# Kernel optimization log

Measured on AMD Instinct MI355X. Metric: run time of the kernel, lower is better.

The kernel has to match this reference:

```python
import jax, jax.numpy as jnp
import numpy as np

B, L = 16, 256
H, NH, NL = 512, 8, 6
NTOK = 10000
P, K = 4, 9          # parser layers, conv kernel size
DFF = 4 * H


def layernorm(x, s=None, b=None, eps=1e-5):
    m = x.mean(-1, keepdims=True)
    v = ((x - m) ** 2).mean(-1, keepdims=True)
    y = (x - m) * jax.lax.rsqrt(v + eps)
    if s is not None:
        y = y * s + b
    return y


def conv1d(h, w, b):
    # h: (B,L,C); w: (K,Cin,Cout); 'same' padding (K odd)
    pad = (K - 1) // 2
    return jax.lax.conv_general_dilated(
        h, w, (1,), [(pad, pad)], dimension_numbers=('NWC', 'WIO', 'NWC')) + b


def setup_inputs():
    key = jax.random.key(0)
    ks = iter(jax.random.split(key, 40))
    r = lambda shape, s=0.02: jax.random.normal(next(ks), shape, jnp.float32) * s
    return dict(
        x=jax.random.randint(next(ks), (B, L), 0, NTOK, jnp.int32),
        pos=jnp.tile(jnp.arange(L, dtype=jnp.int32), (B, 1)),
        emb=r((NTOK, H), 0.1),
        conv_w=r((P, K, H, H)), conv_b=jnp.zeros((P, H)),
        parent_w=r((H, H)), parent_b=jnp.zeros((H,)),
        child_w=r((H, H)), child_b=jnp.zeros((H,)),
        rel_w_param=r((NL, NH, 2), 0.1),
        qkv_w=r((NL, 3 * H, H)), qkv_b=jnp.zeros((NL, 3 * H)),
        out_w=r((NL, H, H)), out_b=jnp.zeros((NL, H)),
        ln1_s=jnp.ones((NL, H)), ln1_b=jnp.zeros((NL, H)),
        ln2_s=jnp.ones((NL, H)), ln2_b=jnp.zeros((NL, H)),
        ff1_w=r((NL, DFF, H)), ff1_b=jnp.zeros((NL, DFF)),
        ff2_w=r((NL, H, DFF)), ff2_b=jnp.zeros((NL, H)),
        norm_s=jnp.ones((H,)), norm_b=jnp.zeros((H,)),
        out_bias=jnp.zeros((NTOK,)),
    )


def _forward(x, floats):
    (emb, conv_w, conv_b, parent_w, parent_b, child_w, child_b, rel_w_param,
     qkv_w, qkv_b, out_w, out_b, ln1_s, ln1_b, ln2_s, ln2_b,
     ff1_w, ff1_b, ff2_w, ff2_b, norm_s, norm_b, out_bias) = floats
    mask = x != 0  # pad token index = 0
    DH = H // NH
    scale = H ** -0.5
    # ---- differentiable parser: Conv1d + LN(no affine) + Tanh stack ----
    h = emb[x]
    for i in range(P):
        h = jnp.where(mask[..., None], h, 0.0)
        h = jnp.tanh(layernorm(conv1d(h, conv_w[i], conv_b[i])))
    parent = h @ parent_w.T + parent_b
    child = h @ child_w.T + child_b
    logits = jnp.einsum('bid,bjd->bij', child, parent) * scale
    logits = jnp.where(mask[:, None, :], logits, -jnp.inf)
    # NB: source applies scaling twice (masked_fill then softmax(logits*scaling))
    p = jax.nn.softmax(logits * scale, axis=-1)  # (B,L,L) head distribution
    # ---- structural relations -> per-layer/per-head attention bias ----
    eye = jnp.eye(L, dtype=bool)
    head = jnp.where(eye, 0.0, p)
    child_rel = jnp.swapaxes(head, 1, 2)
    rel = jnp.stack([head, child_rel], axis=1)            # (B,2,L,L)
    rel_weight = jax.nn.softmax(rel_w_param, axis=-1)     # (NL,NH,2)
    dep = jnp.einsum('lhr,brij->lbhij', rel_weight, rel)  # (NL,B,NH,L,L)
    # ---- pre-LN transformer encoder with structural bias injection ----
    logvis = jnp.where(mask, 0.0, -jnp.inf)[:, None, None, :]  # key padding mask (log)
    h = emb[x]
    for i in range(NL):
        hn = layernorm(h, ln1_s[i], ln1_b[i])
        qkv = hn @ qkv_w[i].T + qkv_b[i]
        q, k, v = jnp.split(qkv, 3, axis=-1)
        split = lambda t: t.reshape(B, L, NH, DH).transpose(0, 2, 1, 3)
        q, k, v = split(q), split(k), split(v)
        att = jnp.einsum('bhid,bhjd->bhij', q, k) * (DH ** -0.5) + dep[i] + logvis
        att = jax.nn.softmax(att, axis=-1)
        ctx = jnp.einsum('bhij,bhjd->bhid', att, v).transpose(0, 2, 1, 3).reshape(B, L, H)
        h = h + ctx @ out_w[i].T + out_b[i]
        hn = layernorm(h, ln2_s[i], ln2_b[i])
        h = h + jax.nn.leaky_relu(hn @ ff1_w[i].T + ff1_b[i], 0.01) @ ff2_w[i].T + ff2_b[i]
    raw = layernorm(h, norm_s, norm_b)
    out = (raw @ emb.T + out_bias).reshape(B * L, NTOK)  # tied output embedding
    return out


def reference(x, pos, emb, conv_w, conv_b, parent_w, parent_b, child_w, child_b,
              rel_w_param, qkv_w, qkv_b, out_w, out_b, ln1_s, ln1_b, ln2_s, ln2_b,
              ff1_w, ff1_b, ff2_w, ff2_b, norm_s, norm_b, out_bias):
    floats = (emb, conv_w, conv_b, parent_w, parent_b, child_w, child_b, rel_w_param,
              qkv_w, qkv_b, out_w, out_b, ln1_s, ln1_b, ln2_s, ln2_b,
              ff1_w, ff1_b, ff2_w, ff2_b, norm_s, norm_b, out_bias)
    return _forward(x, floats)
```

## Files before the change

kernel.cpp:

```cpp
#include <hip/hip_runtime.h>
#include <hip/hip_bf16.h>


typedef unsigned short u16;
typedef unsigned char  u8;
typedef short short8 __attribute__((ext_vector_type(8)));
typedef float f32x4  __attribute__((ext_vector_type(4)));

static constexpr int CB=16, CL=256, CH=512, CNH=8, CDH=64, CNL=6;
static constexpr int CNTOK=10000, CP=4, CKS=9, CDFF=2048, CT=CB*CL;
static constexpr int NTOKP=10112;

__device__ __forceinline__ u16 f2b(float x){
    union { float f; unsigned u; } v; v.f = x;
    unsigned r = v.u + 0x7fffu + ((v.u >> 16) & 1u);
    return (u16)(r >> 16);
}
__device__ __forceinline__ float b2f(u16 u){
    union { unsigned u; float f; } v; v.u = ((unsigned)u) << 16; return v.f;
}
__device__ __forceinline__ unsigned pack2(float a, float b){
    return (unsigned)f2b(a) | ((unsigned)f2b(b) << 16);
}
__device__ __forceinline__ void gll16(const void* g, void* l){
    __builtin_amdgcn_global_load_lds(
        (__attribute__((address_space(1))) void*)g,
        (__attribute__((address_space(3))) void*)l, 16, 0, 0);
}

__global__ __launch_bounds__(256) void cvt_k(const float* __restrict__ in,
    u16* __restrict__ out, long n, long total)
{
    long i = ((long)blockIdx.x * 256 + threadIdx.x) * 8;
    if (i >= total) return;
    uint4 o;
    if (i < n) {
        float4 a = *(const float4*)(in + i);
        float4 b = *(const float4*)(in + i + 4);
        o.x = pack2(a.x, a.y); o.y = pack2(a.z, a.w);
        o.z = pack2(b.x, b.y); o.w = pack2(b.z, b.w);
    } else { o.x = o.y = o.z = o.w = 0u; }
    *(uint4*)(out + i) = o;
}

__global__ __launch_bounds__(256) void embed2_k(const int* __restrict__ x,
    const float* __restrict__ emb, float* __restrict__ h,
    u16* __restrict__ abuf, u8* __restrict__ maskb)
{
    int t = blockIdx.x, tid = threadIdx.x;
    int tok = x[t];
    if (tid == 0) maskb[t] = (tok != 0) ? 1 : 0;
    const float* e = emb + (size_t)tok * CH;
    float v0 = e[tid], v1 = e[tid + 256];
    float* hp = h + (size_t)t * CH;
    hp[tid] = v0; hp[tid + 256] = v1;
    u16* ap = abuf + (size_t)t * CH;
    ap[tid] = f2b(v0); ap[tid + 256] = f2b(v1);
}

template<bool INBF, bool AFFINE, bool DOTANH>
__global__ __launch_bounds__(256) void ln_k(const void* __restrict__ in,
    const float* __restrict__ s, const float* __restrict__ b, u16* __restrict__ out)
{
    int t = blockIdx.x, tid = threadIdx.x;
    float x0, x1;
    if (INBF) {
        const u16* row = (const u16*)in + (size_t)t * CH;
        x0 = b2f(row[tid]); x1 = b2f(row[tid + 256]);
    } else {
        const float* row = (const float*)in + (size_t)t * CH;
        x0 = row[tid]; x1 = row[tid + 256];
    }
    float sum = x0 + x1, sq = x0*x0 + x1*x1;
    #pragma unroll
    for (int o = 32; o; o >>= 1) { sum += __shfl_down(sum, o); sq += __shfl_down(sq, o); }
    __shared__ float rs[4], rq[4];
    int w = tid >> 6, lane = tid & 63;
    if (lane == 0) { rs[w] = sum; rq[w] = sq; }
    __syncthreads();
    sum = rs[0] + rs[1] + rs[2] + rs[3];
    sq  = rq[0] + rq[1] + rq[2] + rq[3];
    float mean = sum * (1.f/512.f);
    float var  = fmaxf(sq * (1.f/512.f) - mean*mean, 0.f);
    float rstd = rsqrtf(var + 1e-5f);
    float y0 = (x0 - mean) * rstd, y1 = (x1 - mean) * rstd;
    if (AFFINE) {
        y0 = y0 * s[tid]       + b[tid];
        y1 = y1 * s[tid + 256] + b[tid + 256];
    }
    if (DOTANH) { y0 = tanhf(y0); y1 = tanhf(y1); }
    u16* o = out + (size_t)t * CH;
    o[tid] = f2b(y0); o[tid + 256] = f2b(y1);
}

__global__ __launch_bounds__(256) void tp_conv(const float* __restrict__ src,
    u16* __restrict__ dst)
{
    __shared__ float tile[32][33];
    int z = blockIdx.z, p = z / 9, t = z % 9;
    int ci0 = blockIdx.y * 32, co0 = blockIdx.x * 32;
    int tx = threadIdx.x, ty = threadIdx.y;
    #pragma unroll
    for (int yy = 0; yy < 4; yy++) {
        int i = ty + yy*8;
        tile[i][tx] = src[((size_t)z*512 + ci0 + i)*512 + co0 + tx];
    }
    __syncthreads();
    #pragma unroll
    for (int yy = 0; yy < 4; yy++) {
        int i = ty + yy*8;
        dst[((size_t)p*512 + co0 + i)*4608 + (size_t)t*512 + ci0 + tx] = f2b(tile[tx][i]);
    }
}

template<int BM, bool CONV, int ACT, int OUT>
__global__ __launch_bounds__(256) void gemm2(
    const u16* __restrict__ A, const u16* __restrict__ B,
    const float* __restrict__ bias, void* __restrict__ Cv,
    const u8* __restrict__ mask,
    int M, int N, int K, float alpha, long sA, long sB, long sC, int swz)
{
    constexpr int MI = BM / 32;
    __shared__ __align__(16) u16 As[32 * BM];
    __shared__ __align__(16) u16 Bs[4096];

    int bx = blockIdx.x, by = blockIdx.y;
    if (swz) {
        int nwg = gridDim.x * gridDim.y;
        int bid = by * gridDim.x + bx;
        int s = (bid & 7) * (nwg >> 3) + (bid >> 3);
        bx = s % gridDim.x; by = s / gridDim.x;
    }
    const int tid  = threadIdx.x;
    const int lane = tid & 63, wave = tid >> 6;
    const int q = lane >> 4, ln = lane & 15;
    const int wm = wave >> 1, wn = wave & 1;
    const int m0 = by * BM, n0 = bx * 128;
    const int z  = blockIdx.z;
    A += (size_t)z * sA; B += (size_t)z * sB;

    f32x4 acc[MI][4];
    #pragma unroll
    for (int i = 0; i < MI; i++)
        #pragma unroll
        for (int j = 0; j < 4; j++)
            #pragma unroll
            for (int r = 0; r < 4; r++) acc[i][j][r] = 0.f;

    for (int k0 = 0; k0 < K; k0 += 32) {
        if (!CONV) {
            if (BM == 128) {
                #pragma unroll
                for (int t = 0; t < 2; t++) {
                    int c = wave + t*4;
                    int kq = c >> 1, rh = (c & 1) << 6;
                    gll16(A + (size_t)(m0 + rh + lane) * K + k0 + kq*8, As + c*512);
                }
            } else {
                gll16(A + (size_t)(m0 + lane) * K + k0 + wave*8, As + wave*512);
            }
        } else {
            int tap = k0 >> 9;
            int ci  = (k0 & 511) + wave*8;
            int gr  = m0 + lane;
            int bb  = gr >> 8;
            int l2  = (gr & 255) + tap - 4;
            bool ok = ((unsigned)l2 < 256u) && mask[(bb << 8) | l2];
            uint4 v; v.x = v.y = v.z = v.w = 0u;
            if (ok) v = *(const uint4*)(A + ((size_t)((bb << 8) | l2)) * CH + ci);
            *(uint4*)&As[wave*512 + lane*8] = v;
        }
        #pragma unroll
        for (int t = 0; t < 2; t++) {
            int c = wave + t*4;
            int kq = c >> 1, rh = (c & 1) << 6;
            gll16(B + (size_t)(n0 + rh + lane) * K + k0 + kq*8, Bs + c*512);
        }
        __syncthreads();
        short8 af[MI], bf[4];
        #pragma unroll
        for (int f = 0; f < MI; f++)
            af[f] = *(const short8*)&As[q*(BM*8) + (wm*(BM/2) + f*16 + ln)*8];
        #pragma unroll
        for (int g = 0; g < 4; g++)
            bf[g] = *(const short8*)&Bs[q*1024 + (wn*64 + g*16 + ln)*8];
        #pragma unroll
        for (int f = 0; f < MI; f++)
            #pragma unroll
            for (int g = 0; g < 4; g++)
                acc[f][g] = __builtin_amdgcn_mfma_f32_16x16x32_bf16(af[f], bf[g], acc[f][g], 0, 0, 0);
        __syncthreads();
    }
    float* Cf = (float*)Cv; u16* Cb = (u16*)Cv;
    #pragma unroll
    for (int f = 0; f < MI; f++) {
        int row0 = m0 + wm*(BM/2) + f*16 + q*4;
        #pragma unroll
        for (int g = 0; g < 4; g++) {
            int col = n0 + wn*64 + g*16 + ln;
            if (col < N) {
                #pragma unroll
                for (int r = 0; r < 4; r++) {
                    float v = acc[f][g][r] * alpha;
                    if (bias) v += bias[col];
                    if (ACT == 1) v = v > 0.f ? v : 0.01f * v;
                    size_t idx = (size_t)z * sC + (size_t)(row0 + r) * N + col;
                    if (OUT == 0)      Cf[idx] = v;
                    else if (OUT == 1) Cb[idx] = f2b(v);
                    else               Cf[idx] += v;
                }
            }
        }
    }
}

__global__ __launch_bounds__(256) void softmax_head(float* __restrict__ sc,
    const u8* __restrict__ mask)
{
    int bi = blockIdx.x;
    int b = bi >> 8, i = bi & 255;
    int j = threadIdx.x;
    float* rowp = sc + (size_t)bi * CL;
    bool valid = mask[(b << 8) | j] != 0;
    float v = valid ? rowp[j] : -1e30f;
    float mx = v;
    #pragma unroll
    for (int o = 32; o; o >>= 1) mx = fmaxf(mx, __shfl_down(mx, o));
    __shared__ float rm[4], rsum[4];
    int w = j >> 6, lane = j & 63;
    if (lane == 0) rm[w] = mx;
    __syncthreads();
    mx = fmaxf(fmaxf(rm[0], rm[1]), fmaxf(rm[2], rm[3]));
    float e = valid ? __expf(v - mx) : 0.f;
    float ssum = e;
    #pragma unroll
    for (int o = 32; o; o >>= 1) ssum += __shfl_down(ssum, o);
    if (lane == 0) rsum[w] = ssum;
    __syncthreads();
    ssum = rsum[0] + rsum[1] + rsum[2] + rsum[3];
    float r = e / fmaxf(ssum, 1e-30f);
    if (j == i) r = 0.f;
    rowp[j] = r;
}

__global__ __launch_bounds__(256) void attn_k(const u16* __restrict__ qkv,
    const float* __restrict__ head, const float* __restrict__ relw,
    const u8* __restrict__ mask, u16* __restrict__ ctx, int layer)
{
    __shared__ __align__(16) u16 Ks[CL * CDH];
    __shared__ __align__(16) u16 Vs[CL * CDH];
    int bx = blockIdx.x;
    int b = bx >> 4, hd = (bx >> 1) & 7, qh = bx & 1;
    int tid = threadIdx.x;

    #pragma unroll
    for (int r = 0; r < 8; r++) {
        int ef = tid + 256 * r;
        int j = ef >> 3, d8 = (ef & 7) * 8;
        const u16* ps = qkv + (size_t)(b*256 + j) * 1536 + 512 + hd*64 + d8;
        *(uint4*)&Ks[j*64 + d8] = *(const uint4*)ps;
        *(uint4*)&Vs[j*64 + d8] = *(const uint4*)(ps + 512);
    }

    int qi = qh * 128 + (tid >> 1);
    int half = tid & 1;
    float qv[CDH];
    {
        const u16* qp = qkv + (size_t)(b*256 + qi) * 1536 + hd*64;
        #pragma unroll
        for (int c = 0; c < 8; c++) {
            uint4 u = *(const uint4*)(qp + c*8);
            unsigned uu[4] = {u.x, u.y, u.z, u.w};
            #pragma unroll
            for (int p2 = 0; p2 < 4; p2++) {
                qv[c*8 + p2*2]     = b2f((u16)(uu[p2] & 0xffffu));
                qv[c*8 + p2*2 + 1] = b2f((u16)(uu[p2] >> 16));
            }
        }
    }
    float r0 = relw[((layer << 3) + hd) * 2 + 0];
    float r1 = relw[((layer << 3) + hd) * 2 + 1];
    float e0 = __expf(r0), e1 = __expf(r1);
    float w0 = e0 / (e0 + e1), w1 = 1.f - w0;

    __syncthreads();

    const float* h1 = head + ((size_t)b << 16) + ((size_t)qi << 8);
    const float* h2 = head + ((size_t)b << 16) + qi;
    const u8* mb = mask + (b << 8);

    float m = -1e30f, lsum = 0.f;
    float acc[CDH];
    #pragma unroll
    for (int d = 0; d < CDH; d++) acc[d] = 0.f;

    for (int jj = 0; jj < 128; jj++) {
        int j = half * 128 + jj;
        if (!mb[j]) continue;
        float dot = 0.f;
        #pragma unroll
        for (int d = 0; d < CDH; d++) dot += qv[d] * b2f(Ks[(j << 6) + d]);
        float s = dot * 0.125f + w0 * h1[j] + w1 * h2[(size_t)j << 8];
        float mn = fmaxf(m, s);
        float c = __expf(m - mn);
        float p = __expf(s - mn);
        lsum = lsum * c + p;
        #pragma unroll
        for (int d = 0; d < CDH; d++) acc[d] = acc[d] * c + p * b2f(Vs[(j << 6) + d]);
        m = mn;
    }
    {
        float mo = __shfl_xor(m, 1);
        float lo = __shfl_xor(lsum, 1);
        float M  = fmaxf(m, mo);
        float cs = __expf(m - M);
        float co = __expf(mo - M);
        lsum = lsum * cs + lo * co;
        #pragma unroll
        for (int d = 0; d < CDH; d++) {
            float ao = __shfl_xor(acc[d], 1);
            acc[d] = acc[d] * cs + ao * co;
        }
    }
    if (half == 0) {
        float inv = 1.f / fmaxf(lsum, 1e-30f);
        u16* cp = ctx + (size_t)(b*256 + qi) * CH + (hd << 6);
        #pragma unroll
        for (int d = 0; d < CDH; d++) cp[d] = f2b(acc[d] * inv);
    }
}

extern "C" void kernel_launch(void* const* d_in, const int* in_sizes, int n_in,
                              void* d_out, int out_size, void* d_ws, size_t ws_size,
                              hipStream_t stream)
{
    const int*   x        = (const int*)d_in[0];
    const float* emb      = (const float*)d_in[2];
    const float* conv_w   = (const float*)d_in[3];
    const float* conv_b   = (const float*)d_in[4];
    const float* parent_w = (const float*)d_in[5];
    const float* parent_b = (const float*)d_in[6];
    const float* child_w  = (const float*)d_in[7];
    const float* child_b  = (const float*)d_in[8];
    const float* rel_w    = (const float*)d_in[9];
    const float* qkv_w    = (const float*)d_in[10];
    const float* qkv_b    = (const float*)d_in[11];
    const float* out_w    = (const float*)d_in[12];
    const float* out_b    = (const float*)d_in[13];
    const float* ln1_s    = (const float*)d_in[14];
    const float* ln1_b    = (const float*)d_in[15];
    const float* ln2_s    = (const float*)d_in[16];
    const float* ln2_b    = (const float*)d_in[17];
    const float* ff1_w    = (const float*)d_in[18];
    const float* ff1_b    = (const float*)d_in[19];
    const float* ff2_w    = (const float*)d_in[20];
    const float* ff2_b    = (const float*)d_in[21];
    const float* norm_s   = (const float*)d_in[22];
    const float* norm_b   = (const float*)d_in[23];
    const float* out_bias = (const float*)d_in[24];

    float* ws = (float*)d_ws;
    float* h      = ws;
    float* headp  = ws + 2097152;
    u16*   abuf   = (u16*)(ws + 3145728);
    u16*   Rb     = (u16*)(ws + 4194304);
    u16*   qkvb   = Rb;
    u16*   parentb= Rb;
    u16*   childb = Rb + 2097152;
    u16*   convo  = Rb + 4194304;
    u16*   ctxb   = (u16*)(ws + 7340032);
    u16*   ff1b   = (u16*)(ws + 8388608);
    u16*   convwb = (u16*)(ws + 7340032);
    u8*    maskb  = (u8*)(ws + 12582912);
    u16*   ebf16  = (u16*)(ws + 12583936);
    u16*   qkvwb  = (u16*)(ws + 15172608);
    u16*   outwb  = (u16*)(ws + 17531904);
    u16*   ff1wb  = (u16*)(ws + 18318336);
    u16*   ff2wb  = (u16*)(ws + 21464064);
    u16*   parwb  = (u16*)(ws + 24609792);
    u16*   chlwb  = (u16*)(ws + 24740864);

    tp_conv<<<dim3(16,16,36), dim3(32,8), 0, stream>>>(conv_w, convwb);
    cvt_k<<<2528, 256, 0, stream>>>(emb,      ebf16, (long)CNTOK*CH, (long)NTOKP*CH);
    cvt_k<<<2304, 256, 0, stream>>>(qkv_w,    qkvwb, 4718592L, 4718592L);
    cvt_k<<< 768, 256, 0, stream>>>(out_w,    outwb, 1572864L, 1572864L);
    cvt_k<<<3072, 256, 0, stream>>>(ff1_w,    ff1wb, 6291456L, 6291456L);
    cvt_k<<<3072, 256, 0, stream>>>(ff2_w,    ff2wb, 6291456L, 6291456L);
    cvt_k<<< 128, 256, 0, stream>>>(parent_w, parwb,  262144L,  262144L);
    cvt_k<<< 128, 256, 0, stream>>>(child_w,  chlwb,  262144L,  262144L);

    embed2_k<<<CT, 256, 0, stream>>>(x, emb, h, abuf, maskb);

    for (int p = 0; p < CP; p++) {
        gemm2<64,true,0,1><<<dim3(4,64,1), 256, 0, stream>>>(
            abuf, convwb + (size_t)p*512*4608, conv_b + p*512, convo, maskb,
            CT, 512, 4608, 1.f, 0, 0, 0, 0);
        ln_k<true,false,true><<<CT, 256, 0, stream>>>(convo, nullptr, nullptr, abuf);
    }
    gemm2<64,false,0,1><<<dim3(4,64,1), 256, 0, stream>>>(
        abuf, parwb, parent_b, parentb, nullptr, CT, 512, 512, 1.f, 0, 0, 0, 0);
    gemm2<64,false,0,1><<<dim3(4,64,1), 256, 0, stream>>>(
        abuf, chlwb, child_b, childb, nullptr, CT, 512, 512, 1.f, 0, 0, 0, 0);
    gemm2<64,false,0,0><<<dim3(2,4,16), 256, 0, stream>>>(
        childb, parentb, nullptr, headp, nullptr, 256, 256, 512, 1.f/512.f,
        131072, 131072, 65536, 0);
    softmax_head<<<CT, 256, 0, stream>>>(headp, maskb);

    for (int l = 0; l < CNL; l++) {
        ln_k<false,true,false><<<CT, 256, 0, stream>>>(h, ln1_s + l*CH, ln1_b + l*CH, abuf);
        gemm2<128,false,0,1><<<dim3(12,32,1), 256, 0, stream>>>(
            abuf, qkvwb + (size_t)l*1536*512, qkv_b + l*1536, qkvb, nullptr,
            CT, 1536, 512, 1.f, 0, 0, 0, 0);
        attn_k<<<256, 256, 0, stream>>>(qkvb, headp, rel_w, maskb, ctxb, l);
        gemm2<64,false,0,2><<<dim3(4,64,1), 256, 0, stream>>>(
            ctxb, outwb + (size_t)l*512*512, out_b + l*512, h, nullptr,
            CT, 512, 512, 1.f, 0, 0, 0, 0);
        ln_k<false,true,false><<<CT, 256, 0, stream>>>(h, ln2_s + l*CH, ln2_b + l*CH, abuf);
        gemm2<128,false,1,1><<<dim3(16,32,1), 256, 0, stream>>>(
            abuf, ff1wb + (size_t)l*2048*512, ff1_b + l*2048, ff1b, nullptr,
            CT, 2048, 512, 1.f, 0, 0, 0, 0);
        gemm2<64,false,0,2><<<dim3(4,64,1), 256, 0, stream>>>(
            ff1b, ff2wb + (size_t)l*512*2048, ff2_b + l*512, h, nullptr,
            CT, 512, 2048, 1.f, 0, 0, 0, 0);
    }
    ln_k<false,true,false><<<CT, 256, 0, stream>>>(h, norm_s, norm_b, abuf);
    gemm2<128,false,0,0><<<dim3(79,32,1), 256, 0, stream>>>(
        abuf, ebf16, out_bias, d_out, nullptr, CT, CNTOK, 512, 1.f, 0, 0, 0, 1);
}
```

Measured before the change: 2.595 ms.

## Pad conv input, transpose head matrix, split-K residual GEMMs, column-major swizzle

The conv input now lives in a zero-padded per-batch buffer with masked rows zeroed at write time. The conv GEMM can then load A tiles with direct global-to-LDS copies, with no bounds or mask checks. The head matrix is transposed once so attention reads its second term contiguously instead of with a 256-float stride. The out-proj and FF2 GEMMs use 2-way split-K with atomic adds into the residual to double the block count. Several GEMMs also switch to a different block swizzle. The transposed head buffer borrows the output buffer as scratch, and the atomics make the summation order nondeterministic.

```diff
diff --git a/kernel.cpp b/kernel.cpp
--- a/kernel.cpp
+++ b/kernel.cpp
@@ -10,6 +10,7 @@
 static constexpr int CB=16, CL=256, CH=512, CNH=8, CDH=64, CNL=6;
 static constexpr int CNTOK=10000, CP=4, CKS=9, CDFF=2048, CT=CB*CL;
 static constexpr int NTOKP=10112;
+static constexpr int LP=264;
 
 __device__ __forceinline__ u16 f2b(float x){
     union { float f; unsigned u; } v; v.f = x;
@@ -45,22 +46,26 @@
 
 __global__ __launch_bounds__(256) void embed2_k(const int* __restrict__ x,
     const float* __restrict__ emb, float* __restrict__ h,
-    u16* __restrict__ abuf, u8* __restrict__ maskb)
+    u16* __restrict__ ppad, u8* __restrict__ maskb)
 {
     int t = blockIdx.x, tid = threadIdx.x;
     int tok = x[t];
-    if (tid == 0) maskb[t] = (tok != 0) ? 1 : 0;
+    bool mk = (tok != 0);
+    if (tid == 0) maskb[t] = mk ? 1 : 0;
     const float* e = emb + (size_t)tok * CH;
     float v0 = e[tid], v1 = e[tid + 256];
     float* hp = h + (size_t)t * CH;
     hp[tid] = v0; hp[tid + 256] = v1;
-    u16* ap = abuf + (size_t)t * CH;
-    ap[tid] = f2b(v0); ap[tid + 256] = f2b(v1);
-}
-
-template<bool INBF, bool AFFINE, bool DOTANH>
+    int pr = (t >> 8) * LP + 4 + (t & 255);
+    u16* ap = ppad + (size_t)pr * CH;
+    ap[tid]       = mk ? f2b(v0) : (u16)0;
+    ap[tid + 256] = mk ? f2b(v1) : (u16)0;
+}
+
+template<bool INBF, bool AFFINE, bool DOTANH, int OUTMODE>
 __global__ __launch_bounds__(256) void ln_k(const void* __restrict__ in,
-    const float* __restrict__ s, const float* __restrict__ b, u16* __restrict__ out)
+    const float* __restrict__ s, const float* __restrict__ b, u16* __restrict__ out,
+    const u8* __restrict__ mask)
 {
     int t = blockIdx.x, tid = threadIdx.x;
     float x0, x1;
@@ -89,8 +94,16 @@
         y1 = y1 * s[tid + 256] + b[tid + 256];
     }
     if (DOTANH) { y0 = tanhf(y0); y1 = tanhf(y1); }
-    u16* o = out + (size_t)t * CH;
-    o[tid] = f2b(y0); o[tid + 256] = f2b(y1);
+    if (OUTMODE == 0) {
+        u16* o = out + (size_t)t * CH;
+        o[tid] = f2b(y0); o[tid + 256] = f2b(y1);
+    } else {
+        bool mk = mask[t] != 0;
+        int pr = (t >> 8) * LP + 4 + (t & 255);
+        u16* o = out + (size_t)pr * CH;
+        o[tid]       = mk ? f2b(y0) : (u16)0;
+        o[tid + 256] = mk ? f2b(y1) : (u16)0;
+    }
 }
 
 __global__ __launch_bounds__(256) void tp_conv(const float* __restrict__ src,
@@ -113,11 +126,30 @@
     }
 }
 
-template<int BM, bool CONV, int ACT, int OUT>
+__global__ __launch_bounds__(256) void tp_head(const float* __restrict__ src,
+    float* __restrict__ dst)
+{
+    __shared__ float tile[32][33];
+    int b = blockIdx.z;
+    int i0 = blockIdx.y * 32, j0 = blockIdx.x * 32;
+    int tx = threadIdx.x & 31, ty = threadIdx.x >> 5;
+    #pragma unroll
+    for (int yy = 0; yy < 4; yy++) {
+        int i = ty + yy*8;
+        tile[i][tx] = src[((size_t)b*256 + i0 + i)*256 + j0 + tx];
+    }
+    __syncthreads();
+    #pragma unroll
+    for (int yy = 0; yy < 4; yy++) {
+        int i = ty + yy*8;
+        dst[((size_t)b*256 + j0 + i)*256 + i0 + tx] = tile[tx][i];
+    }
+}
+
+template<int BM, bool CONV, int ACT, int OUT, int SPLITK>
 __global__ __launch_bounds__(256) void gemm2(
     const u16* __restrict__ A, const u16* __restrict__ B,
     const float* __restrict__ bias, void* __restrict__ Cv,
-    const u8* __restrict__ mask,
     int M, int N, int K, float alpha, long sA, long sB, long sC, int swz)
 {
     constexpr int MI = BM / 32;
@@ -128,8 +160,9 @@
     if (swz) {
         int nwg = gridDim.x * gridDim.y;
         int bid = by * gridDim.x + bx;
-        int s = (bid & 7) * (nwg >> 3) + (bid >> 3);
-        bx = s % gridDim.x; by = s / gridDim.x;
+        bid = (bid & 7) * (nwg >> 3) + (bid >> 3);
+        if (swz == 2) { by = bid % gridDim.y; bx = bid / gridDim.y; }
+        else          { bx = bid % gridDim.x; by = bid / gridDim.x; }
     }
     const int tid  = threadIdx.x;
     const int lane = tid & 63, wave = tid >> 6;
@@ -137,7 +170,14 @@
     const int wm = wave >> 1, wn = wave & 1;
     const int m0 = by * BM, n0 = bx * 128;
     const int z  = blockIdx.z;
-    A += (size_t)z * sA; B += (size_t)z * sB;
+
+    int kbeg = 0, kend = K;
+    if (SPLITK > 1) {
+        int ks = K / SPLITK;
+        kbeg = z * ks; kend = kbeg + ks;
+    } else {
+        A += (size_t)z * sA; B += (size_t)z * sB;
+    }
 
     f32x4 acc[MI][4];
     #pragma unroll
@@ -147,28 +187,22 @@
             #pragma unroll
             for (int r = 0; r < 4; r++) acc[i][j][r] = 0.f;
 
-    for (int k0 = 0; k0 < K; k0 += 32) {
-        if (!CONV) {
-            if (BM == 128) {
-                #pragma unroll
-                for (int t = 0; t < 2; t++) {
-                    int c = wave + t*4;
-                    int kq = c >> 1, rh = (c & 1) << 6;
-                    gll16(A + (size_t)(m0 + rh + lane) * K + k0 + kq*8, As + c*512);
-                }
-            } else {
-                gll16(A + (size_t)(m0 + lane) * K + k0 + wave*8, As + wave*512);
-            }
-        } else {
+    for (int k0 = kbeg; k0 < kend; k0 += 32) {
+        if (CONV) {
             int tap = k0 >> 9;
             int ci  = (k0 & 511) + wave*8;
             int gr  = m0 + lane;
-            int bb  = gr >> 8;
-            int l2  = (gr & 255) + tap - 4;
-            bool ok = ((unsigned)l2 < 256u) && mask[(bb << 8) | l2];
-            uint4 v; v.x = v.y = v.z = v.w = 0u;
-            if (ok) v = *(const uint4*)(A + ((size_t)((bb << 8) | l2)) * CH + ci);
-            *(uint4*)&As[wave*512 + lane*8] = v;
+            int pr  = (gr >> 8) * LP + (gr & 255) + tap;
+            gll16(A + (size_t)pr * CH + ci, As + wave*512);
+        } else if (BM == 128) {
+            #pragma unroll
+            for (int t = 0; t < 2; t++) {
+                int c = wave + t*4;
+                int kq = c >> 1, rh = (c & 1) << 6;
+                gll16(A + (size_t)(m0 + rh + lane) * K + k0 + kq*8, As + c*512);
+            }
+        } else {
+            gll16(A + (size_t)(m0 + lane) * K + k0 + wave*8, As + wave*512);
         }
         #pragma unroll
         for (int t = 0; t < 2; t++) {
@@ -192,6 +226,8 @@
         __syncthreads();
     }
     float* Cf = (float*)Cv; u16* Cb = (u16*)Cv;
+    size_t zoff = (SPLITK > 1) ? 0 : (size_t)z * sC;
+    bool addb = bias && (SPLITK == 1 || z == 0);
     #pragma unroll
     for (int f = 0; f < MI; f++) {
         int row0 = m0 + wm*(BM/2) + f*16 + q*4;
@@ -202,12 +238,13 @@
                 #pragma unroll
                 for (int r = 0; r < 4; r++) {
                     float v = acc[f][g][r] * alpha;
-                    if (bias) v += bias[col];
+                    if (addb) v += bias[col];
                     if (ACT == 1) v = v > 0.f ? v : 0.01f * v;
-                    size_t idx = (size_t)z * sC + (size_t)(row0 + r) * N + col;
+                    size_t idx = zoff + (size_t)(row0 + r) * N + col;
                     if (OUT == 0)      Cf[idx] = v;
                     else if (OUT == 1) Cb[idx] = f2b(v);
-                    else               Cf[idx] += v;
+                    else if (OUT == 2) Cf[idx] += v;
+                    else               atomicAdd(&Cf[idx], v);
                 }
             }
         }
@@ -244,8 +281,9 @@
 }
 
 __global__ __launch_bounds__(256) void attn_k(const u16* __restrict__ qkv,
-    const float* __restrict__ head, const float* __restrict__ relw,
-    const u8* __restrict__ mask, u16* __restrict__ ctx, int layer)
+    const float* __restrict__ head, const float* __restrict__ headT,
+    const float* __restrict__ relw, const u8* __restrict__ mask,
+    u16* __restrict__ ctx, int layer)
 {
     __shared__ __align__(16) u16 Ks[CL * CDH];
     __shared__ __align__(16) u16 Vs[CL * CDH];
@@ -285,8 +323,8 @@
 
     __syncthreads();
 
-    const float* h1 = head + ((size_t)b << 16) + ((size_t)qi << 8);
-    const float* h2 = head + ((size_t)b << 16) + qi;
+    const float* h1 = head  + ((size_t)b << 16) + ((size_t)qi << 8);
+    const float* h2 = headT + ((size_t)b << 16) + ((size_t)qi << 8);
     const u8* mb = mask + (b << 8);
 
     float m = -1e30f, lsum = 0.f;
@@ -300,7 +338,7 @@
         float dot = 0.f;
         #pragma unroll
         for (int d = 0; d < CDH; d++) dot += qv[d] * b2f(Ks[(j << 6) + d]);
-        float s = dot * 0.125f + w0 * h1[j] + w1 * h2[(size_t)j << 8];
+        float s = dot * 0.125f + w0 * h1[j] + w1 * h2[j];
         float mn = fmaxf(m, s);
         float c = __expf(m - mn);
         float p = __expf(s - mn);
@@ -365,6 +403,7 @@
     u16*   abuf   = (u16*)(ws + 3145728);
     u16*   Rb     = (u16*)(ws + 4194304);
     u16*   qkvb   = Rb;
+    u16*   ppad   = Rb;
     u16*   parentb= Rb;
     u16*   childb = Rb + 2097152;
     u16*   convo  = Rb + 4194304;
@@ -379,6 +418,7 @@
     u16*   ff2wb  = (u16*)(ws + 21464064);
     u16*   parwb  = (u16*)(ws + 24609792);
     u16*   chlwb  = (u16*)(ws + 24740864);
+    float* headT  = (float*)d_out;
 
     tp_conv<<<dim3(16,16,36), dim3(32,8), 0, stream>>>(conv_w, convwb);
     cvt_k<<<2528, 256, 0, stream>>>(emb,      ebf16, (long)CNTOK*CH, (long)NTOKP*CH);
@@ -389,41 +429,45 @@
     cvt_k<<< 128, 256, 0, stream>>>(parent_w, parwb,  262144L,  262144L);
     cvt_k<<< 128, 256, 0, stream>>>(child_w,  chlwb,  262144L,  262144L);
 
-    embed2_k<<<CT, 256, 0, stream>>>(x, emb, h, abuf, maskb);
-
+    hipMemsetAsync(ppad, 0, (size_t)CB * LP * CH * 2, stream);
+    embed2_k<<<CT, 256, 0, stream>>>(x, emb, h, ppad, maskb);
     for (int p = 0; p < CP; p++) {
-        gemm2<64,true,0,1><<<dim3(4,64,1), 256, 0, stream>>>(
-            abuf, convwb + (size_t)p*512*4608, conv_b + p*512, convo, maskb,
-            CT, 512, 4608, 1.f, 0, 0, 0, 0);
-        ln_k<true,false,true><<<CT, 256, 0, stream>>>(convo, nullptr, nullptr, abuf);
-    }
-    gemm2<64,false,0,1><<<dim3(4,64,1), 256, 0, stream>>>(
-        abuf, parwb, parent_b, parentb, nullptr, CT, 512, 512, 1.f, 0, 0, 0, 0);
-    gemm2<64,false,0,1><<<dim3(4,64,1), 256, 0, stream>>>(
-        abuf, chlwb, child_b, childb, nullptr, CT, 512, 512, 1.f, 0, 0, 0, 0);
-    gemm2<64,false,0,0><<<dim3(2,4,16), 256, 0, stream>>>(
-        childb, parentb, nullptr, headp, nullptr, 256, 256, 512, 1.f/512.f,
+        gemm2<64,true,0,1,1><<<dim3(4,64,1), 256, 0, stream>>>(
+            ppad, convwb + (size_t)p*512*4608, conv_b + p*512, convo,
+            CT, 512, 4608, 1.f, 0, 0, 0, 2);
+        if (p < CP-1)
+            ln_k<true,false,true,1><<<CT, 256, 0, stream>>>(convo, nullptr, nullptr, ppad, maskb);
+        else
+            ln_k<true,false,true,0><<<CT, 256, 0, stream>>>(convo, nullptr, nullptr, abuf, nullptr);
+    }
+    gemm2<64,false,0,1,1><<<dim3(4,64,1), 256, 0, stream>>>(
+        abuf, parwb, parent_b, parentb, CT, 512, 512, 1.f, 0, 0, 0, 2);
+    gemm2<64,false,0,1,1><<<dim3(4,64,1), 256, 0, stream>>>(
+        abuf, chlwb, child_b, childb, CT, 512, 512, 1.f, 0, 0, 0, 2);
+    gemm2<64,false,0,0,1><<<dim3(2,4,16), 256, 0, stream>>>(
+        childb, parentb, nullptr, headp, 256, 256, 512, 1.f/512.f,
         131072, 131072, 65536, 0);
     softmax_head<<<CT, 256, 0, stream>>>(headp, maskb);
+    tp_head<<<dim3(8,8,16), 256, 0, stream>>>(headp, headT);
 
     for (int l = 0; l < CNL; l++) {
-        ln_k<false,true,false><<<CT, 256, 0, stream>>>(h, ln1_s + l*CH, ln1_b + l*CH, abuf);
-        gemm2<128,false,0,1><<<dim3(12,32,1), 256, 0, stream>>>(
-            abuf, qkvwb + (size_t)l*1536*512, qkv_b + l*1536, qkvb, nullptr,
-            CT, 1536, 512, 1.f, 0, 0, 0, 0);
-        attn_k<<<256, 256, 0, stream>>>(qkvb, headp, rel_w, maskb, ctxb, l);
-        gemm2<64,false,0,2><<<dim3(4,64,1), 256, 0, stream>>>(
-            ctxb, outwb + (size_t)l*512*512, out_b + l*512, h, nullptr,
-            CT, 512, 512, 1.f, 0, 0, 0, 0);
-        ln_k<false,true,false><<<CT, 256, 0, stream>>>(h, ln2_s + l*CH, ln2_b + l*CH, abuf);
-        gemm2<128,false,1,1><<<dim3(16,32,1), 256, 0, stream>>>(
-            abuf, ff1wb + (size_t)l*2048*512, ff1_b + l*2048, ff1b, nullptr,
-            CT, 2048, 512, 1.f, 0, 0, 0, 0);
-        gemm2<64,false,0,2><<<dim3(4,64,1), 256, 0, stream>>>(
-            ff1b, ff2wb + (size_t)l*512*2048, ff2_b + l*512, h, nullptr,
-            CT, 512, 2048, 1.f, 0, 0, 0, 0);
-    }
-    ln_k<false,true,false><<<CT, 256, 0, stream>>>(h, norm_s, norm_b, abuf);
-    gemm2<128,false,0,0><<<dim3(79,32,1), 256, 0, stream>>>(
-        abuf, ebf16, out_bias, d_out, nullptr, CT, CNTOK, 512, 1.f, 0, 0, 0, 1);
-}
+        ln_k<false,true,false,0><<<CT, 256, 0, stream>>>(h, ln1_s + l*CH, ln1_b + l*CH, abuf, nullptr);
+        gemm2<128,false,0,1,1><<<dim3(12,32,1), 256, 0, stream>>>(
+            abuf, qkvwb + (size_t)l*1536*512, qkv_b + l*1536, qkvb,
+            CT, 1536, 512, 1.f, 0, 0, 0, 1);
+        attn_k<<<256, 256, 0, stream>>>(qkvb, headp, headT, rel_w, maskb, ctxb, l);
+        gemm2<64,false,0,3,2><<<dim3(4,64,2), 256, 0, stream>>>(
+            ctxb, outwb + (size_t)l*512*512, out_b + l*512, h,
+            CT, 512, 512, 1.f, 0, 0, 0, 2);
+        ln_k<false,true,false,0><<<CT, 256, 0, stream>>>(h, ln2_s + l*CH, ln2_b + l*CH, abuf, nullptr);
+        gemm2<128,false,1,1,1><<<dim3(16,32,1), 256, 0, stream>>>(
+            abuf, ff1wb + (size_t)l*2048*512, ff1_b + l*2048, ff1b,
+            CT, 2048, 512, 1.f, 0, 0, 0, 1);
+        gemm2<64,false,0,3,2><<<dim3(4,64,2), 256, 0, stream>>>(
+            ff1b, ff2wb + (size_t)l*512*2048, ff2_b + l*512, h,
+            CT, 512, 2048, 1.f, 0, 0, 0, 2);
+    }
+    ln_k<false,true,false,0><<<CT, 256, 0, stream>>>(h, norm_s, norm_b, abuf, nullptr);
+    gemm2<128,false,0,0,1><<<dim3(79,32,1), 256, 0, stream>>>(
+        abuf, ebf16, out_bias, d_out, CT, CNTOK, 512, 1.f, 0, 0, 0, 2);
+}
```

Result: faster. 2.511 ms (-3.2%).
